# Optimization experiments

Hardware: AMD Instinct MI355X
Metric: run time of the kernel (lower is better)

Reference implementation:

```python
import jax, jax.numpy as jnp
from jax import lax
import numpy as np

# Layer dims: (in, hidden) for encoder 1-3 and decoder 1-3
INPUT_SIZE = 64
HIDDEN_SIZE = 16
LAYER_DIMS = [
    ("e1", INPUT_SIZE, 48), ("e2", 48, 32), ("e3", 32, HIDDEN_SIZE),
    ("d1", HIDDEN_SIZE, 32), ("d2", 32, 48), ("d3", 48, INPUT_SIZE),
]


def _lstm_layer(x, Wih, Whh, bih, bhh):
    """PyTorch-convention single-layer LSTM (gate order i,f,g,o), batch_first.
    x: [B,T,D], Wih: [4H,D], Whh: [4H,H], biases: [4H].
    Returns (outputs [B,T,H], last_h [B,H])."""
    B, T, _ = x.shape
    H = Whh.shape[1]
    # Precompute input contribution to all gates for all timesteps (one big GEMM).
    xg = jnp.einsum('btd,gd->btg', x, Wih) + (bih + bhh)  # [B,T,4H]

    def step(carry, xt):
        h, c = carry
        g = xt + h @ Whh.T                      # [B,4H]
        i, f, gg, o = jnp.split(g, 4, axis=-1)
        i = jax.nn.sigmoid(i)
        f = jax.nn.sigmoid(f)
        gg = jnp.tanh(gg)
        o = jax.nn.sigmoid(o)
        c = f * c + i * gg
        h = o * jnp.tanh(c)
        return (h, c), h

    h0 = jnp.zeros((B, H), x.dtype)
    (hT, _), ys = lax.scan(step, (h0, h0), jnp.swapaxes(xg, 0, 1))
    return jnp.swapaxes(ys, 0, 1), hT


def setup_inputs() -> dict:
    key = jax.random.key(0)
    B, T = 512, 512
    k_x, key = jax.random.split(key)
    inp = {"x": jax.random.normal(k_x, (B, T, INPUT_SIZE), dtype=jnp.float32)}
    for name, din, dh in LAYER_DIMS:
        bound = 1.0 / np.sqrt(dh)  # PyTorch nn.LSTM init: U(-1/sqrt(H), 1/sqrt(H))
        for suf, shape in [("Wih", (4 * dh, din)), ("Whh", (4 * dh, dh)),
                           ("bih", (4 * dh,)), ("bhh", (4 * dh,))]:
            key, k = jax.random.split(key)
            inp[f"{name}_{suf}"] = jax.random.uniform(
                k, shape, minval=-bound, maxval=bound, dtype=jnp.float32)
    return inp


def reference(x,
              e1_Wih, e1_Whh, e1_bih, e1_bhh,
              e2_Wih, e2_Whh, e2_bih, e2_bhh,
              e3_Wih, e3_Whh, e3_bih, e3_bhh,
              d1_Wih, d1_Whh, d1_bih, d1_bhh,
              d2_Wih, d2_Whh, d2_bih, d2_bhh,
              d3_Wih, d3_Whh, d3_bih, d3_bhh):
    # Encoder
    z, _ = _lstm_layer(x, e1_Wih, e1_Whh, e1_bih, e1_bhh)
    z, _ = _lstm_layer(z, e2_Wih, e2_Whh, e2_bih, e2_bhh)
    _, last_h = _lstm_layer(z, e3_Wih, e3_Whh, e3_bih, e3_bhh)
    # Repeat latent across time: [B,H] -> [B,T,H]
    T = x.shape[1]
    x_enc = jnp.broadcast_to(last_h[:, None, :], (x.shape[0], T, last_h.shape[-1]))
    # Decoder
    z, _ = _lstm_layer(x_enc, d1_Wih, d1_Whh, d1_bih, d1_bhh)
    z, _ = _lstm_layer(z, d2_Wih, d2_Whh, d2_bih, d2_bhh)
    x_dec, _ = _lstm_layer(z, d3_Wih, d3_Whh, d3_bih, d3_bhh)
    return x_dec
```

## Files before the change

kernel.cpp:

```cpp
#include <hip/hip_runtime.h>
#include <hip/hip_bf16.h>
#include <cstdint>
#include <cstddef>

typedef _Float16 half_t;
typedef decltype(__builtin_amdgcn_cvt_pkrtz(0.f, 0.f)) h2;

__device__ __forceinline__ h2 pk2(float a, float b) { return __builtin_amdgcn_cvt_pkrtz(a, b); }
__device__ __forceinline__ float fdot2f(h2 a, h2 b, float c) { return __builtin_amdgcn_fdot2(a, b, c, false); }
__device__ __forceinline__ h2 u2h(uint32_t u) { union { uint32_t u; h2 h; } v; v.u = u; return v.h; }

#define WAVE_SYNC() asm volatile("s_waitcnt lgkmcnt(0)" ::: "memory")
#define BLOCK_SYNC()                                   \
  do {                                                 \
    asm volatile("s_waitcnt lgkmcnt(0)" ::: "memory"); \
    __builtin_amdgcn_s_barrier();                      \
    asm volatile("" ::: "memory");                     \
  } while (0)

template <int NQ>
__device__ __forceinline__ void fetch_q(const half_t* hb, uint4* q) {
  const uint4* p = (const uint4*)hb;
#pragma unroll
  for (int i = 0; i < NQ; ++i) q[i] = p[i];
}

template <int NQ>
__device__ __forceinline__ void dot4(const h2* w, const uint4* q, float* a) {
#pragma unroll
  for (int i = 0; i < NQ; ++i) {
    a[0] = fdot2f(w[4 * i + 0], u2h(q[i].x), a[0]);
    a[1] = fdot2f(w[4 * i + 1], u2h(q[i].y), a[1]);
    a[2] = fdot2f(w[4 * i + 2], u2h(q[i].z), a[2]);
    a[3] = fdot2f(w[4 * i + 3], u2h(q[i].w), a[3]);
  }
}

__device__ __forceinline__ void load_row_h2(const float* src, int nf, h2* dst) {
  const float2* s2 = (const float2*)src;
  for (int p = 0; p < nf / 2; ++p) { float2 v = s2[p]; dst[p] = pk2(v.x, v.y); }
}

__device__ __forceinline__ void gconst(int gt, float& s, float& a, float& b) {
  const bool isT = (gt == 2);
  s = isT ? -2.88539008f : -1.44269504f;
  a = isT ? 2.f : 1.f;
  b = isT ? -1.f : 0.f;
}

__device__ __forceinline__ float act_sig(float x) {
  float e = exp2f(-1.44269504f * x);
  return __builtin_amdgcn_rcpf(1.f + e);
}
__device__ __forceinline__ float act_tanh(float x) {
  float e = exp2f(-2.88539008f * x);
  return fmaf(2.f, __builtin_amdgcn_rcpf(1.f + e), -1.f);
}
__device__ __forceinline__ float act_rt(float x, float s, float a, float b) {
  float e = exp2f(s * x);
  return fmaf(a, __builtin_amdgcn_rcpf(1.f + e), b);
}

__device__ __forceinline__ float comb4(float gi, float gf, float gg, float go, float& c) {
  c = fmaf(gf, c, gi * gg);
  float e2 = exp2f(-2.88539008f * c);
  return go * fmaf(2.f, __builtin_amdgcn_rcpf(1.f + e2), -1.f);
}

__device__ __forceinline__ float pair_combine(float gv0, float gv1, int l, float& c) {
  float sw0 = __shfl_xor(gv0, 32, 64);
  float sw1 = __shfl_xor(gv1, 32, 64);
  const bool lo = (l < 32);
  float gi = lo ? gv0 : sw0, gf = lo ? gv1 : sw1;
  float gg = lo ? sw0 : gv0, go = lo ? sw1 : gv1;
  return comb4(gi, gf, gg, go, c);
}

__global__ __launch_bounds__(256, 2) void ae_ker(
    const float* __restrict__ W0, const float* __restrict__ U0, const float* __restrict__ b0i, const float* __restrict__ b0h,
    const float* __restrict__ W1, const float* __restrict__ U1, const float* __restrict__ b1i, const float* __restrict__ b1h,
    const float* __restrict__ W2, const float* __restrict__ U2, const float* __restrict__ b2i, const float* __restrict__ b2h,
    const float* __restrict__ W3, const float* __restrict__ U3, const float* __restrict__ b3i, const float* __restrict__ b3h,
    const float* __restrict__ W4, const float* __restrict__ U4, const float* __restrict__ b4i, const float* __restrict__ b4h,
    const float* __restrict__ W5, const float* __restrict__ U5, const float* __restrict__ b5i, const float* __restrict__ b5h,
    const float* __restrict__ x, float* __restrict__ out, int T) {
  __shared__ __align__(16) half_t hb1e[2][48];
  __shared__ __align__(16) half_t hb2e[2][32];
  __shared__ __align__(16) half_t hb3e[2][16];
  __shared__ __align__(16) uint32_t xrow16[2][32];
  __shared__ __align__(16) float xg1[2][192];
  __shared__ __align__(16) float latb[16];
  __shared__ __align__(16) half_t hb1d[2][32];
  __shared__ __align__(16) half_t hb2d[2][48];
  __shared__ __align__(16) half_t hb3d[2][64];
  __shared__ __align__(16) float xg2[2][192];

  const int tid = threadIdx.x, wv = tid >> 6, l = tid & 63, b = blockIdx.x;
  const int uu = (l < 48) ? l : 47;

  if (tid < 48) { hb1e[0][tid] = (half_t)0.f; hb1e[1][tid] = (half_t)0.f; }
  if (tid < 32) { hb2e[0][tid] = (half_t)0.f; hb2e[1][tid] = (half_t)0.f; }
  if (tid < 16) { hb3e[0][tid] = (half_t)0.f; hb3e[1][tid] = (half_t)0.f; }

  h2 w[112];
  float bias[3] = {0.f, 0.f, 0.f};
  float bx[3] = {0.f, 0.f, 0.f};
  float sA[2], aA[2], bB[2];
  float c = 0.f;
  float2 va = {0.f, 0.f}, vb = {0.f, 0.f};
  const float2* xp = nullptr;

  if (wv == 0) {
#pragma unroll
    for (int j = 0; j < 4; ++j)
      load_row_h2(U0 + (size_t)(j * 48 + uu) * 48, 48, w + j * 24);
  } else if (wv == 1) {
    const int u = l & 31, g0 = (l < 32) ? 0 : 2;
#pragma unroll
    for (int j = 0; j < 2; ++j) {
      const int r = (g0 + j) * 32 + u;
      load_row_h2(W1 + (size_t)r * 48, 48, w + j * 40);
      load_row_h2(U1 + (size_t)r * 32, 32, w + j * 40 + 24);
      bias[j] = b1i[r] + b1h[r];
      gconst(g0 + j, sA[j], aA[j], bB[j]);
    }
  } else if (wv == 2) {
    load_row_h2(W2 + (size_t)l * 32, 32, w);
    load_row_h2(U2 + (size_t)l * 16, 16, w + 16);
    bias[0] = b2i[l] + b2h[l];
    gconst(l >> 4, sA[0], aA[0], bB[0]);
  } else {
#pragma unroll
    for (int j = 0; j < 3; ++j) {
      const int r = 64 * j + l;
      load_row_h2(W0 + (size_t)r * 64, 64, w + j * 32);
      bias[j] = b0i[r] + b0h[r];
    }
    xp = (const float2*)(x + (size_t)b * T * 64) + (l & 31);
    if (l < 32) {
      float2 x0 = xp[0], x1 = xp[32];
      union { h2 h; uint32_t u; } c0, c1;
      c0.h = pk2(x0.x, x0.y);
      c1.h = pk2(x1.x, x1.y);
      xrow16[0][l] = c0.u;
      xrow16[1][l] = c1.u;
      va = xp[64];
      vb = xp[96];
    }
    WAVE_SYNC();
    uint4 xq[8];
    const uint4* xr = (const uint4*)&xrow16[0][0];
#pragma unroll
    for (int i = 0; i < 8; ++i) xq[i] = xr[i];
#pragma unroll
    for (int j = 0; j < 3; ++j) {
      float a[4] = {bias[j], 0.f, 0.f, 0.f};
      dot4<8>(w + j * 32, xq, a);
      xg1[0][64 * j + l] = (a[0] + a[1]) + (a[2] + a[3]);
    }
  }
  BLOCK_SYNC();

  auto estep = [&](const bool G, int s, int P) {
    const int Q = P ^ 1;
    if (wv == 0) {
      if (!G || s < T) {
        float xgv[4];
#pragma unroll
        for (int j = 0; j < 4; ++j) xgv[j] = xg1[P][j * 48 + uu];
        uint4 hq[6];
        fetch_q<6>(&hb1e[Q][0], hq);
        __builtin_amdgcn_s_setprio(1);
        float gv[4];
#pragma unroll
        for (int j = 0; j < 4; ++j) {
          float a[4] = {xgv[j], 0.f, 0.f, 0.f};
          dot4<6>(w + j * 24, hq, a);
          float pre = (a[0] + a[1]) + (a[2] + a[3]);
          gv[j] = (j == 2) ? act_tanh(pre) : act_sig(pre);
        }
        __builtin_amdgcn_s_setprio(0);
        float h = comb4(gv[0], gv[1], gv[2], gv[3], c);
        if (l < 48) hb1e[P][l] = (half_t)h;
      }
    } else if (wv == 1) {
      if (!G || (s >= 1 && s <= T)) {
        uint4 xv[6], hq[4];
        fetch_q<6>(&hb1e[Q][0], xv);
        fetch_q<4>(&hb2e[Q][0], hq);
        float gv[2];
#pragma unroll
        for (int j = 0; j < 2; ++j) {
          float a[4] = {bias[j], 0.f, 0.f, 0.f};
          dot4<6>(w + j * 40, xv, a);
          dot4<4>(w + j * 40 + 24, hq, a);
          gv[j] = act_rt((a[0] + a[1]) + (a[2] + a[3]), sA[j], aA[j], bB[j]);
        }
        float h = pair_combine(gv[0], gv[1], l, c);
        if (l < 32) hb2e[P][l & 31] = (half_t)h;
      }
    } else if (wv == 2) {
      if (!G || s >= 2) {
        uint4 xv[4], hq[2];
        fetch_q<4>(&hb2e[Q][0], xv);
        fetch_q<2>(&hb3e[Q][0], hq);
        float a[4] = {bias[0], 0.f, 0.f, 0.f};
        dot4<4>(w, xv, a);
        dot4<2>(w + 16, hq, a);
        float gvv = act_rt((a[0] + a[1]) + (a[2] + a[3]), sA[0], aA[0], bB[0]);
        float s1 = __shfl_xor(gvv, 16, 64);
        float r0 = __shfl_xor(gvv, 32, 64);
        float r1 = __shfl_xor(s1, 32, 64);
        float h = comb4(gvv, s1, r0, r1, c);
        if (l < 16) {
          hb3e[P][l] = (half_t)h;
          if (G && s - 2 == T - 1) latb[l] = h;
        }
      }
    } else {
      if ((!G || s + 2 < T) && l < 32) {
        union { h2 h; uint32_t u; } cc2;
        float2 v = P ? vb : va;
        cc2.h = pk2(v.x, v.y);
        xrow16[P][l] = cc2.u;
        if (!G || s + 4 < T) {
          float2 nv = xp[(size_t)(s + 4) * 32];
          if (P) vb = nv; else va = nv;
        }
      }
      if (!G || s + 1 < T) {
        WAVE_SYNC();
        uint4 xq[8];
        const uint4* xr = (const uint4*)&xrow16[Q][0];
#pragma unroll
        for (int i = 0; i < 8; ++i) xq[i] = xr[i];
        __builtin_amdgcn_s_setprio(1);
#pragma unroll
        for (int j = 0; j < 3; ++j) {
          float a[4] = {bias[j], 0.f, 0.f, 0.f};
          dot4<8>(w + j * 32, xq, a);
          xg1[Q][64 * j + l] = (a[0] + a[1]) + (a[2] + a[3]);
        }
        __builtin_amdgcn_s_setprio(0);
      }
    }
    BLOCK_SYNC();
  };

  {
    const int NS = T + 2;
    for (int s = 0; s < 4; ++s) estep(true, s, s & 1);
    for (int s = 4; s < 508; s += 2) { estep(false, s, 0); estep(false, s + 1, 1); }
    for (int s = 508; s < NS; ++s) estep(true, s, s & 1);
  }

  c = 0.f;
  if (tid < 32) { hb1d[0][tid] = (half_t)0.f; hb1d[1][tid] = (half_t)0.f; }
  if (tid < 48) { hb2d[0][tid] = (half_t)0.f; hb2d[1][tid] = (half_t)0.f; }
  if (tid < 64) { hb3d[0][tid] = (half_t)0.f; hb3d[1][tid] = (half_t)0.f; }
  const int u2 = (l & 31) + ((wv == 3) ? 32 : 0);

  if (wv == 0) {
    const int u = l & 31, g0 = (l < 32) ? 0 : 2;
#pragma unroll
    for (int j = 0; j < 2; ++j) {
      const int r = (g0 + j) * 32 + u;
      load_row_h2(U3 + (size_t)r * 32, 32, w + j * 16);
      float s0 = b3i[r] + b3h[r];
      const float* wr = W3 + (size_t)r * 16;
#pragma unroll
      for (int d = 0; d < 16; ++d) s0 = fmaf(wr[d], latb[d], s0);
      bias[j] = s0;
      gconst(g0 + j, sA[j], aA[j], bB[j]);
    }
#pragma unroll
    for (int jj = 0; jj < 3; ++jj) {
      const int r = 64 * jj + l;
      load_row_h2(W4 + (size_t)r * 32, 32, w + 32 + jj * 16);
      bx[jj] = b4i[r] + b4h[r];
    }
  } else if (wv == 1) {
#pragma unroll
    for (int j = 0; j < 4; ++j)
      load_row_h2(U4 + (size_t)(j * 48 + uu) * 48, 48, w + j * 24);
  } else {
    const int g0 = (l < 32) ? 0 : 2;
#pragma unroll
    for (int j = 0; j < 2; ++j) {
      const int r = (g0 + j) * 64 + u2;
      load_row_h2(W5 + (size_t)r * 48, 48, w + j * 56);
      load_row_h2(U5 + (size_t)r * 64, 64, w + j * 56 + 24);
      bias[j] = b5i[r] + b5h[r];
      gconst(g0 + j, sA[j], aA[j], bB[j]);
    }
  }
  BLOCK_SYNC();

  auto dstep = [&](const bool G, int s, int P) {
    const int Q = P ^ 1;
    if (wv == 0) {
      if (!G || s <= T) {
        uint4 hq[4];
        fetch_q<4>(&hb1d[Q][0], hq);
        if (!G || s < T) {
          float gv[2];
#pragma unroll
          for (int j = 0; j < 2; ++j) {
            float a[4] = {bias[j], 0.f, 0.f, 0.f};
            dot4<4>(w + j * 16, hq, a);
            gv[j] = act_rt((a[0] + a[1]) + (a[2] + a[3]), sA[j], aA[j], bB[j]);
          }
          float h = pair_combine(gv[0], gv[1], l, c);
          if (l < 32) hb1d[P][l & 31] = (half_t)h;
        }
        if (!G || s >= 1) {
#pragma unroll
          for (int jj = 0; jj < 3; ++jj) {
            float a[4] = {bx[jj], 0.f, 0.f, 0.f};
            dot4<4>(w + 32 + jj * 16, hq, a);
            xg2[P][64 * jj + l] = (a[0] + a[1]) + (a[2] + a[3]);
          }
        }
      }
    } else if (wv == 1) {
      if (!G || (s >= 2 && s < T + 2)) {
        float xgv[4];
#pragma unroll
        for (int j = 0; j < 4; ++j) xgv[j] = xg2[Q][j * 48 + uu];
        uint4 hq[6];
        fetch_q<6>(&hb2d[Q][0], hq);
        __builtin_amdgcn_s_setprio(1);
        float gv[4];
#pragma unroll
        for (int j = 0; j < 4; ++j) {
          float a[4] = {xgv[j], 0.f, 0.f, 0.f};
          dot4<6>(w + j * 24, hq, a);
          float pre = (a[0] + a[1]) + (a[2] + a[3]);
          gv[j] = (j == 2) ? act_tanh(pre) : act_sig(pre);
        }
        __builtin_amdgcn_s_setprio(0);
        float h = comb4(gv[0], gv[1], gv[2], gv[3], c);
        if (l < 48) hb2d[P][l] = (half_t)h;
      }
    } else {
      if (!G || (s >= 3 && s < T + 3)) {
        uint4 xv[6], hq[8];
        fetch_q<6>(&hb2d[Q][0], xv);
        fetch_q<8>(&hb3d[Q][0], hq);
        __builtin_amdgcn_s_setprio(1);
        float gv[2];
#pragma unroll
        for (int j = 0; j < 2; ++j) {
          float a[4] = {bias[j], 0.f, 0.f, 0.f};
          dot4<6>(w + j * 56, xv, a);
          dot4<8>(w + j * 56 + 24, hq, a);
          gv[j] = act_rt((a[0] + a[1]) + (a[2] + a[3]), sA[j], aA[j], bB[j]);
        }
        __builtin_amdgcn_s_setprio(0);
        float h = pair_combine(gv[0], gv[1], l, c);
        if (l < 32) {
          hb3d[P][u2] = (half_t)h;
          out[((size_t)b * T + (s - 3)) * 64 + u2] = h;
        }
      }
    }
    BLOCK_SYNC();
  };

  {
    const int NS = T + 4;
    for (int s = 0; s < 4; ++s) dstep(true, s, s & 1);
    for (int s = 4; s < 508; s += 2) { dstep(false, s, 0); dstep(false, s + 1, 1); }
    for (int s = 508; s < NS; ++s) dstep(true, s, s & 1);
  }
}

extern "C" void kernel_launch(void* const* d_in, const int* in_sizes, int n_in,
                              void* d_out, int out_size, void* d_ws, size_t ws_size,
                              hipStream_t stream) {
  (void)in_sizes; (void)n_in; (void)out_size; (void)d_ws; (void)ws_size;
  const float* x = (const float*)d_in[0];
  const float *W[6], *U[6], *Bi[6], *Bh[6];
  for (int lyr = 0; lyr < 6; ++lyr) {
    W[lyr]  = (const float*)d_in[1 + 4 * lyr + 0];
    U[lyr]  = (const float*)d_in[1 + 4 * lyr + 1];
    Bi[lyr] = (const float*)d_in[1 + 4 * lyr + 2];
    Bh[lyr] = (const float*)d_in[1 + 4 * lyr + 3];
  }
  float* out = (float*)d_out;
  const int T = 512;

  ae_ker<<<dim3(512), dim3(256), 0, stream>>>(
      W[0], U[0], Bi[0], Bh[0], W[1], U[1], Bi[1], Bh[1], W[2], U[2], Bi[2], Bh[2],
      W[3], U[3], Bi[3], Bh[3], W[4], U[4], Bi[4], Bh[4], W[5], U[5], Bi[5], Bh[5],
      x, out, T);
}
```

Measured before the change: 723.7 us.

## Rebalance encoder input-projection work onto wave 2 and rotate wave roles per block

New measurement: 752.6 us. 4.0% more time.

```diff
diff --git a/kernel.cpp b/kernel.cpp
--- a/kernel.cpp
+++ b/kernel.cpp
@@ -96,6 +96,8 @@
   __shared__ __align__(16) float xg2[2][192];
 
   const int tid = threadIdx.x, wv = tid >> 6, l = tid & 63, b = blockIdx.x;
+  const int par = ((b >> 8) ^ b) & 1;
+  const int role = (wv + (par << 1)) & 3;
   const int uu = (l < 48) ? l : 47;
 
   if (tid < 48) { hb1e[0][tid] = (half_t)0.f; hb1e[1][tid] = (half_t)0.f; }
@@ -110,11 +112,11 @@
   float2 va = {0.f, 0.f}, vb = {0.f, 0.f};
   const float2* xp = nullptr;
 
-  if (wv == 0) {
+  if (role == 0) {
 #pragma unroll
     for (int j = 0; j < 4; ++j)
       load_row_h2(U0 + (size_t)(j * 48 + uu) * 48, 48, w + j * 24);
-  } else if (wv == 1) {
+  } else if (role == 1) {
     const int u = l & 31, g0 = (l < 32) ? 0 : 2;
 #pragma unroll
     for (int j = 0; j < 2; ++j) {
@@ -124,14 +126,16 @@
       bias[j] = b1i[r] + b1h[r];
       gconst(g0 + j, sA[j], aA[j], bB[j]);
     }
-  } else if (wv == 2) {
+  } else if (role == 2) {
     load_row_h2(W2 + (size_t)l * 32, 32, w);
     load_row_h2(U2 + (size_t)l * 16, 16, w + 16);
     bias[0] = b2i[l] + b2h[l];
     gconst(l >> 4, sA[0], aA[0], bB[0]);
+    load_row_h2(W0 + (size_t)(128 + l) * 64, 64, w + 24);
+    bx[0] = b0i[128 + l] + b0h[128 + l];
   } else {
 #pragma unroll
-    for (int j = 0; j < 3; ++j) {
+    for (int j = 0; j < 2; ++j) {
       const int r = 64 * j + l;
       load_row_h2(W0 + (size_t)r * 64, 64, w + j * 32);
       bias[j] = b0i[r] + b0h[r];
@@ -147,23 +151,31 @@
       va = xp[64];
       vb = xp[96];
     }
+  }
+  if (role == 3) {
     WAVE_SYNC();
     uint4 xq[8];
-    const uint4* xr = (const uint4*)&xrow16[0][0];
-#pragma unroll
-    for (int i = 0; i < 8; ++i) xq[i] = xr[i];
-#pragma unroll
-    for (int j = 0; j < 3; ++j) {
+    fetch_q<8>((const half_t*)&xrow16[0][0], xq);
+#pragma unroll
+    for (int j = 0; j < 2; ++j) {
       float a[4] = {bias[j], 0.f, 0.f, 0.f};
       dot4<8>(w + j * 32, xq, a);
       xg1[0][64 * j + l] = (a[0] + a[1]) + (a[2] + a[3]);
     }
   }
   BLOCK_SYNC();
+  if (role == 2) {
+    uint4 xq[8];
+    fetch_q<8>((const half_t*)&xrow16[0][0], xq);
+    float a[4] = {bx[0], 0.f, 0.f, 0.f};
+    dot4<8>(w + 24, xq, a);
+    xg1[0][128 + l] = (a[0] + a[1]) + (a[2] + a[3]);
+  }
+  BLOCK_SYNC();
 
   auto estep = [&](const bool G, int s, int P) {
     const int Q = P ^ 1;
-    if (wv == 0) {
+    if (role == 0) {
       if (!G || s < T) {
         float xgv[4];
 #pragma unroll
@@ -183,7 +195,7 @@
         float h = comb4(gv[0], gv[1], gv[2], gv[3], c);
         if (l < 48) hb1e[P][l] = (half_t)h;
       }
-    } else if (wv == 1) {
+    } else if (role == 1) {
       if (!G || (s >= 1 && s <= T)) {
         uint4 xv[6], hq[4];
         fetch_q<6>(&hb1e[Q][0], xv);
@@ -199,7 +211,7 @@
         float h = pair_combine(gv[0], gv[1], l, c);
         if (l < 32) hb2e[P][l & 31] = (half_t)h;
       }
-    } else if (wv == 2) {
+    } else if (role == 2) {
       if (!G || s >= 2) {
         uint4 xv[4], hq[2];
         fetch_q<4>(&hb2e[Q][0], xv);
@@ -217,6 +229,13 @@
           if (G && s - 2 == T - 1) latb[l] = h;
         }
       }
+      if (!G || s + 1 < T) {
+        uint4 xq[8];
+        fetch_q<8>((const half_t*)&xrow16[Q][0], xq);
+        float a[4] = {bx[0], 0.f, 0.f, 0.f};
+        dot4<8>(w + 24, xq, a);
+        xg1[Q][128 + l] = (a[0] + a[1]) + (a[2] + a[3]);
+      }
     } else {
       if ((!G || s + 2 < T) && l < 32) {
         union { h2 h; uint32_t u; } cc2;
@@ -231,12 +250,10 @@
       if (!G || s + 1 < T) {
         WAVE_SYNC();
         uint4 xq[8];
-        const uint4* xr = (const uint4*)&xrow16[Q][0];
-#pragma unroll
-        for (int i = 0; i < 8; ++i) xq[i] = xr[i];
+        fetch_q<8>((const half_t*)&xrow16[Q][0], xq);
         __builtin_amdgcn_s_setprio(1);
 #pragma unroll
-        for (int j = 0; j < 3; ++j) {
+        for (int j = 0; j < 2; ++j) {
           float a[4] = {bias[j], 0.f, 0.f, 0.f};
           dot4<8>(w + j * 32, xq, a);
           xg1[Q][64 * j + l] = (a[0] + a[1]) + (a[2] + a[3]);
@@ -258,9 +275,9 @@
   if (tid < 32) { hb1d[0][tid] = (half_t)0.f; hb1d[1][tid] = (half_t)0.f; }
   if (tid < 48) { hb2d[0][tid] = (half_t)0.f; hb2d[1][tid] = (half_t)0.f; }
   if (tid < 64) { hb3d[0][tid] = (half_t)0.f; hb3d[1][tid] = (half_t)0.f; }
-  const int u2 = (l & 31) + ((wv == 3) ? 32 : 0);
-
-  if (wv == 0) {
+  const int u2 = (l & 31) + ((role == 3) ? 32 : 0);
+
+  if (role == 0) {
     const int u = l & 31, g0 = (l < 32) ? 0 : 2;
 #pragma unroll
     for (int j = 0; j < 2; ++j) {
@@ -279,7 +296,7 @@
       load_row_h2(W4 + (size_t)r * 32, 32, w + 32 + jj * 16);
       bx[jj] = b4i[r] + b4h[r];
     }
-  } else if (wv == 1) {
+  } else if (role == 1) {
 #pragma unroll
     for (int j = 0; j < 4; ++j)
       load_row_h2(U4 + (size_t)(j * 48 + uu) * 48, 48, w + j * 24);
@@ -298,7 +315,7 @@
 
   auto dstep = [&](const bool G, int s, int P) {
     const int Q = P ^ 1;
-    if (wv == 0) {
+    if (role == 0) {
       if (!G || s <= T) {
         uint4 hq[4];
         fetch_q<4>(&hb1d[Q][0], hq);
@@ -322,7 +339,7 @@
           }
         }
       }
-    } else if (wv == 1) {
+    } else if (role == 1) {
       if (!G || (s >= 2 && s < T + 2)) {
         float xgv[4];
 #pragma unroll
```
